# Kernel optimization log

Hardware: AMD Instinct MI355X
Metric: run time of the kernel (lower is better)

Reference implementation:

```python
import jax, jax.numpy as jnp
import numpy as np

B, A, C, G = 32, 5, 20, 19
TPER = 8  # targets per image -> T = B*TPER = 256
ANCHORS = np.array([[1.3221, 1.73145], [3.19275, 4.00944], [5.05587, 8.09892],
                    [9.47112, 4.84053], [11.2364, 10.0071]], dtype=np.float32)
OBJECT_SCALE, NOOBJECT_SCALE, CLASS_SCALE, COORD_SCALE = 5.0, 1.0, 1.0, 1.0
THRESH = 0.6


def _wh_iou_np(anc, wh):
    inter = np.minimum(anc[:, 0:1], wh[None, :, 0]) * np.minimum(anc[:, 1:2], wh[None, :, 1])
    union = anc[:, 0:1] * anc[:, 1:2] + wh[None, :, 0] * wh[None, :, 1] - inter
    return inter / (union + 1e-16)


def setup_inputs() -> dict:
    rng = np.random.default_rng(0)
    rows = []
    for b in range(B):
        cells = rng.choice(G * G, TPER, replace=False)  # distinct grid cells per image
        for c in cells:
            gy, gx = divmod(int(c), G)
            u, v = rng.uniform(0.05, 0.95, 2)
            w, h = rng.uniform(1.0, 8.0, 2) / G  # 1..8 grid units, in 0..1 image coords
            rows.append([b, rng.integers(C), (gx + u) / G, (gy + v) / G, w, h])
    t = np.array(rows, dtype=np.float32)
    # sort targets into (sample, anchor, gy, gx) mask order so mask-order gathers
    # line up with target-row order (as the original torch code implicitly assumes)
    wh_g = t[:, 4:6] * G
    ai = np.argmax(_wh_iou_np(ANCHORS, wh_g), axis=0)
    gx = (t[:, 2] * G).astype(np.int64)
    gy = (t[:, 3] * G).astype(np.int64)
    flat = ((t[:, 0].astype(np.int64) * A + ai) * G + gy) * G + gx
    t = t[np.argsort(flat)]
    x = jax.random.normal(jax.random.key(0), (B, A * (C + 5), G, G), dtype=jnp.float32) * 0.5
    return {"x": x, "targets": jnp.asarray(t), "seen": 0}


def _bbox_iou(b1, b2):
    # center-format boxes, last dim = (x, y, w, h); broadcasts over leading dims
    b1x1 = b1[..., 0] - b1[..., 2] / 2; b1x2 = b1[..., 0] + b1[..., 2] / 2
    b1y1 = b1[..., 1] - b1[..., 3] / 2; b1y2 = b1[..., 1] + b1[..., 3] / 2
    b2x1 = b2[..., 0] - b2[..., 2] / 2; b2x2 = b2[..., 0] + b2[..., 2] / 2
    b2y1 = b2[..., 1] - b2[..., 3] / 2; b2y2 = b2[..., 1] + b2[..., 3] / 2
    iw = jnp.clip(jnp.minimum(b1x2, b2x2) - jnp.maximum(b1x1, b2x1), 0.0)
    ih = jnp.clip(jnp.minimum(b1y2, b2y2) - jnp.maximum(b1y1, b2y1), 0.0)
    inter = iw * ih
    union = b1[..., 2] * b1[..., 3] + b2[..., 2] * b2[..., 3] - inter
    return inter / (union + 1e-16)


def _forward(x, targets, seen):
    anchors = jnp.asarray(ANCHORS)
    xp = x.reshape(B, A, C + 5, G, G).transpose(0, 1, 3, 4, 2)  # (B,A,G,G,C+5)
    tx, ty, tw, th = xp[..., 0], xp[..., 1], xp[..., 2], xp[..., 3]
    pred_conf = jax.nn.sigmoid(xp[..., 4])
    pred_cls = jax.nn.sigmoid(xp[..., 5:])
    tgs = targets[:, 2:6] * G  # (T,4) in grid units
    # anchor assignment via wh-iou (argmax over anchors)
    inter = jnp.minimum(anchors[:, 0:1], tgs[None, :, 2]) * jnp.minimum(anchors[:, 1:2], tgs[None, :, 3])
    wh_iou = inter / (anchors[:, 0:1] * anchors[:, 1:2] + tgs[None, :, 2] * tgs[None, :, 3] - inter)
    ai = jnp.argmax(wh_iou, axis=0)
    gx = tgs[:, 0].astype(jnp.int32); gy = tgs[:, 1].astype(jnp.int32)
    si = targets[:, 0].astype(jnp.int32); ci = targets[:, 1].astype(jnp.int32)
    # decode full grid
    gridx = jnp.arange(G, dtype=x.dtype)[None, None, None, :]
    gridy = jnp.arange(G, dtype=x.dtype)[None, None, :, None]
    sx, sy = jax.nn.sigmoid(tx), jax.nn.sigmoid(ty)
    pw = jnp.exp(tw) * anchors[:, 0][None, :, None, None]
    ph = jnp.exp(th) * anchors[:, 1][None, :, None, None]
    pred_boxes = jnp.stack([sx + gridx, sy + gridy, pw, ph], axis=-1)  # (B,A,G,G,4)
    T = targets.shape[0]
    target_mask = jnp.zeros((B, A, G, G), bool).at[si, ai, gy, gx].set(True)
    # losses at the T target locations (targets pre-sorted into mask order)
    iou_t = _bbox_iou(pred_boxes[si, ai, gy, gx], tgs)  # (T,)
    loss_cls = jnp.mean((pred_cls[si, ai, gy, gx] - jax.nn.one_hot(ci, C, dtype=x.dtype)) ** 2) * CLASS_SCALE
    tconf = iou_t  # rescore == 1: target_conf = 1 * iou
    loss_obj = jnp.mean((pred_conf[si, ai, gy, gx] - tconf) ** 2) * OBJECT_SCALE
    tcoords = jnp.stack([tgs[:, 0] - gx, tgs[:, 1] - gy,
                         jnp.log(tgs[:, 2] / anchors[ai, 0]),
                         jnp.log(tgs[:, 3] / anchors[ai, 1])], axis=-1)  # (T,4)
    pcoords_t = jnp.stack([sx[si, ai, gy, gx], sy[si, ai, gy, gx],
                           tw[si, ai, gy, gx], th[si, ai, gy, gx]], axis=-1)
    scale = jnp.sqrt(2.0 - tgs[:, 2] * tgs[:, 3] / (G * G))[:, None]
    loss_coords = jnp.mean(((pcoords_t - tcoords) * scale) ** 2) * COORD_SCALE
    # noobject mask: any-target IoU > thresh suppresses the noobj penalty (chunked over targets)
    CHUNK = 32
    tchunks = tgs.reshape(T // CHUNK, CHUNK, 4)
    def body(mx, tc):
        iou = _bbox_iou(pred_boxes[None], tc[:, None, None, None, None, :])  # (CHUNK,B,A,G,G)
        return jnp.maximum(mx, iou.max(0)), None
    max_iou, _ = jax.lax.scan(body, jnp.zeros((B, A, G, G), x.dtype), tchunks)
    noobj = (~target_mask) & (max_iou <= THRESH)
    ncnt = jnp.sum(noobj)
    loss_noobj = jnp.sum(jnp.where(noobj, pred_conf ** 2, 0.0)) / ncnt * NOOBJECT_SCALE
    total = loss_cls + loss_obj + loss_coords + loss_noobj
    if seen < 12800:
        prior = jnp.array([0.5, 0.5, 0.0, 0.0], x.dtype)
        pcoords = jnp.stack([sx, sy, tw, th], axis=-1)  # (B,A,G,G,4)
        nm = ~target_mask
        loss_prior = jnp.sum(jnp.where(nm[..., None], (pcoords - prior) ** 2, 0.0)) / (jnp.sum(nm) * 4) * 0.01
        total = total + loss_prior
    return total


def reference(x, targets, seen):
    return _forward(x, targets, seen)
```

## Files before the change

### kernel.cpp

```cpp
#include <hip/hip_runtime.h>
#include <math.h>

#define NB 32
#define NA 5
#define NC 20
#define NG 19
#define NT 256
#define GG  (NG*NG)
#define CELLS (NB*NA*NG*NG)
#define CPB 64
#define NBLK ((CELLS + CPB - 1)/CPB)
#define NWAVE 8
#define NTHR (NWAVE*64)

#define OBJECT_SCALE   5.0f
#define NOOBJ_SCALE    1.0f
#define CLASS_SCALE    1.0f
#define COORD_SCALE    1.0f

__constant__ float c_aw[5] = {1.3221f, 3.19275f, 5.05587f, 9.47112f, 11.2364f};
__constant__ float c_ah[5] = {1.73145f, 4.00944f, 8.09892f, 4.84053f, 10.0071f};

__device__ __forceinline__ float sigm(float v) { return 1.f / (1.f + expf(-v)); }

#define SUMS_OFF 0
#define PART_OFF 16

__global__ __launch_bounds__(NTHR)
void k_main(const float* __restrict__ x, const float* __restrict__ tg,
            float* __restrict__ ws_f, float* __restrict__ partials) {
    __shared__ float4 s_corn[NT];
    __shared__ float  s_s06[NT];
    __shared__ int    s_mask[CPB];
    __shared__ float  s_pm[NWAVE][CPB];
    __shared__ float  s_wred[12];

    const int t = threadIdx.x;
    const int wave = t >> 6, lane = t & 63;
    const int cellBase = blockIdx.x * CPB;
    const int idx = cellBase + lane;
    const bool valid = idx < CELLS;

    float txv = 0.f, tyv = 0.f, twv = 0.f, thv = 0.f, cfv = 0.f;
    int ca = 0, cgx = 0, cgy = 0;
    if (valid) {
        int gx = idx % NG;
        int r  = idx / NG;
        int gy = r % NG;  r /= NG;
        int a  = r % NA;
        int b  = r / NA;
        ca = a; cgx = gx; cgy = gy;
        int base = ((b*NA + a)*(NC+5))*GG + gy*NG + gx;
        txv = x[base + 0*GG];
        tyv = x[base + 1*GG];
        twv = x[base + 2*GG];
        thv = x[base + 3*GG];
        cfv = x[base + 4*GG];
    }
    if (t < CPB) s_mask[t] = 0;

    float gxf = 0.f, gyf = 0.f, gw = 0.f, gh = 0.f;
    int si = 0, ci = 0, ai = 0, gxi = 0, gyi = 0, fid = -1;
    if (t < NT) {
        const float2* tg2 = (const float2*)tg;
        float2 p0 = tg2[t*3+0], p1 = tg2[t*3+1], p2 = tg2[t*3+2];
        gxf = p1.x * NG; gyf = p1.y * NG;
        gw  = p2.x * NG; gh  = p2.y * NG;
        si = (int)p0.x; ci = (int)p0.y;
        float tarea = gw * gh;
        float b_inter = fminf(c_aw[0], gw) * fminf(c_ah[0], gh);
        float b_uni   = c_aw[0]*c_ah[0] + tarea - b_inter;
        #pragma unroll
        for (int a = 1; a < NA; ++a) {
            float inter = fminf(c_aw[a], gw) * fminf(c_ah[a], gh);
            float uni   = c_aw[a]*c_ah[a] + tarea - inter;
            if (inter * b_uni > b_inter * uni) { b_inter = inter; b_uni = uni; ai = a; }
        }
        gxi = (int)gxf; gyi = (int)gyf;
        fid = ((si*NA + ai)*NG + gyi)*NG + gxi;
        float hw = gw*0.5f, hh = gh*0.5f;
        s_corn[t] = make_float4(gxf - hw, gyf - hh, gxf + hw, gyf + hh);
        s_s06[t]  = 0.6f * tarea;
    }
    __syncthreads();

    if (t < NT) {
        int rel = fid - cellBase;
        if (rel >= 0 && rel < CPB) s_mask[rel] = 1;
    }
    float bx1 = 1e30f, by1 = 1e30f, bx2 = 1e30f, by2 = 1e30f, cthr = 0.f;
    float sx = 0.f, sy = 0.f;
    if (valid) {
        sx = sigm(txv); sy = sigm(tyv);
        float pw = expf(twv) * c_aw[ca], ph = expf(thv) * c_ah[ca];
        float cx = sx + (float)cgx, cy = sy + (float)cgy;
        bx1 = cx - pw*0.5f; bx2 = cx + pw*0.5f;
        by1 = cy - ph*0.5f; by2 = cy + ph*0.5f;
        cthr = 0.6f * (pw * ph) + 6e-17f;
    }
    __syncthreads();

    float m0 = -1e30f, m1 = -1e30f;
    #pragma unroll
    for (int i = 0; i < 16; ++i) {
        int j0 = (i << 4) + wave;
        int j1 = j0 + 8;
        float4 ta = s_corn[j0];
        float sa = s_s06[j0];
        float4 tb = s_corn[j1];
        float sb = s_s06[j1];
        float iwa = fmaxf(fminf(bx2, ta.z) - fmaxf(bx1, ta.x), 0.f);
        float iha = fmaxf(fminf(by2, ta.w) - fmaxf(by1, ta.y), 0.f);
        float iwb = fmaxf(fminf(bx2, tb.z) - fmaxf(bx1, tb.x), 0.f);
        float ihb = fmaxf(fminf(by2, tb.w) - fmaxf(by1, tb.y), 0.f);
        m0 = fmaxf(m0, fmaf(1.6f, iwa * iha, -sa));
        m1 = fmaxf(m1, fmaf(1.6f, iwb * ihb, -sb));
    }
    s_pm[wave][lane] = fmaxf(m0, m1);
    __syncthreads();

    if (wave == 0) {
        float mm = s_pm[0][lane];
        #pragma unroll
        for (int w = 1; w < NWAVE; ++w) mm = fmaxf(mm, s_pm[w][lane]);
        float v_no = 0.f, v_nc = 0.f, v_pr = 0.f, v_nm = 0.f;
        if (valid && !s_mask[lane]) {
            v_nm = 1.f;
            float e0 = sx - 0.5f, e1 = sy - 0.5f;
            v_pr = e0*e0 + e1*e1 + twv*twv + thv*thv;
            if (!(mm > cthr)) {
                float pc = sigm(cfv);
                v_no = pc * pc;
                v_nc = 1.f;
            }
        }
        #pragma unroll
        for (int off = 32; off > 0; off >>= 1) {
            v_no += __shfl_down(v_no, off);
            v_nc += __shfl_down(v_nc, off);
            v_pr += __shfl_down(v_pr, off);
            v_nm += __shfl_down(v_nm, off);
        }
        if (lane == 0) {
            partials[blockIdx.x*4 + 0] = v_no;
            partials[blockIdx.x*4 + 1] = v_nc;
            partials[blockIdx.x*4 + 2] = v_pr;
            partials[blockIdx.x*4 + 3] = v_nm;
        }
    }

    if (blockIdx.x == 0) {
        float s_cls = 0.f, s_obj = 0.f, s_crd = 0.f;
        if (t < NT) {
            int base = ((si*NA + ai)*(NC+5))*GG + gyi*NG + gxi;
            float txt = x[base + 0*GG];
            float tyt = x[base + 1*GG];
            float twt = x[base + 2*GG];
            float tht = x[base + 3*GG];
            float cft = x[base + 4*GG];
            float tsx = sigm(txt), tsy = sigm(tyt);
            float aw = c_aw[ai], ah = c_ah[ai];
            float pw = expf(twt) * aw, ph = expf(tht) * ah;

            float pcx = tsx + (float)gxi, pcy = tsy + (float)gyi;
            float hw = gw*0.5f, hh = gh*0.5f;
            float iw = fmaxf(0.f, fminf(pcx + pw*0.5f, gxf + hw) - fmaxf(pcx - pw*0.5f, gxf - hw));
            float ih = fmaxf(0.f, fminf(pcy + ph*0.5f, gyf + hh) - fmaxf(pcy - ph*0.5f, gyf - hh));
            float inter = iw * ih;
            float uni = pw*ph + gw*gh - inter;
            float iou = inter / (uni + 1e-16f);

            float pconf = sigm(cft);
            float dobj = pconf - iou;
            s_obj = dobj * dobj;

            for (int cc = 0; cc < NC; ++cc) {
                float pc = sigm(x[base + (5 + cc)*GG]);
                float d = pc - ((cc == ci) ? 1.f : 0.f);
                s_cls += d * d;
            }

            float scl = sqrtf(2.f - gw*gh / (float)(NG*NG));
            float d0 = (tsx - (gxf - (float)gxi)) * scl;
            float d1 = (tsy - (gyf - (float)gyi)) * scl;
            float d2 = (twt - logf(gw / aw)) * scl;
            float d3 = (tht - logf(gh / ah)) * scl;
            s_crd = d0*d0 + d1*d1 + d2*d2 + d3*d3;

            #pragma unroll
            for (int off = 32; off > 0; off >>= 1) {
                s_cls += __shfl_down(s_cls, off);
                s_obj += __shfl_down(s_obj, off);
                s_crd += __shfl_down(s_crd, off);
            }
            if (lane == 0) {
                s_wred[wave*3 + 0] = s_cls;
                s_wred[wave*3 + 1] = s_obj;
                s_wred[wave*3 + 2] = s_crd;
            }
        }
        __syncthreads();
        if (t == 0) {
            ws_f[SUMS_OFF + 0] = s_wred[0] + s_wred[3] + s_wred[6] + s_wred[9];
            ws_f[SUMS_OFF + 1] = s_wred[1] + s_wred[4] + s_wred[7] + s_wred[10];
            ws_f[SUMS_OFF + 2] = s_wred[2] + s_wred[5] + s_wred[8] + s_wred[11];
        }
    }
}

__global__ __launch_bounds__(256)
void k_final(const float* __restrict__ ws_f, const float* __restrict__ partials,
             const int* __restrict__ seen, float* __restrict__ out) {
    const float4* p4 = (const float4*)partials;
    int t = threadIdx.x;
    float a0 = 0.f, a1 = 0.f, a2 = 0.f, a3 = 0.f;
    for (int j = t; j < NBLK; j += 256) {
        float4 v = p4[j];
        a0 += v.x; a1 += v.y; a2 += v.z; a3 += v.w;
    }
    #pragma unroll
    for (int off = 32; off > 0; off >>= 1) {
        a0 += __shfl_down(a0, off);
        a1 += __shfl_down(a1, off);
        a2 += __shfl_down(a2, off);
        a3 += __shfl_down(a3, off);
    }
    __shared__ float s_w[4][4];
    int wave = t >> 6, lane = t & 63;
    if (lane == 0) {
        s_w[wave][0] = a0; s_w[wave][1] = a1; s_w[wave][2] = a2; s_w[wave][3] = a3;
    }
    __syncthreads();
    if (t == 0) {
        float r0 = s_w[0][0] + s_w[1][0] + s_w[2][0] + s_w[3][0];
        float r1 = s_w[0][1] + s_w[1][1] + s_w[2][1] + s_w[3][1];
        float r2 = s_w[0][2] + s_w[1][2] + s_w[2][2] + s_w[3][2];
        float r3 = s_w[0][3] + s_w[1][3] + s_w[2][3] + s_w[3][3];
        float loss_cls = ws_f[SUMS_OFF + 0] / (float)(NT * NC) * CLASS_SCALE;
        float loss_obj = ws_f[SUMS_OFF + 1] / (float)NT * OBJECT_SCALE;
        float loss_crd = ws_f[SUMS_OFF + 2] / (float)(NT * 4) * COORD_SCALE;
        float loss_no  = r0 / r1 * NOOBJ_SCALE;
        float total = loss_cls + loss_obj + loss_crd + loss_no;
        if (seen[0] < 12800) {
            total += r2 / (r3 * 4.f) * 0.01f;
        }
        out[0] = total;
    }
}

extern "C" void kernel_launch(void* const* d_in, const int* in_sizes, int n_in,
                              void* d_out, int out_size, void* d_ws, size_t ws_size,
                              hipStream_t stream) {
    const float* x    = (const float*)d_in[0];
    const float* tg   = (const float*)d_in[1];
    const int*   seen = (const int*)d_in[2];
    float* out  = (float*)d_out;
    float* ws_f = (float*)d_ws;
    float* partials = ws_f + PART_OFF;

    k_main<<<NBLK, NTHR, 0, stream>>>(x, tg, ws_f, partials);
    k_final<<<1, 256, 0, stream>>>(ws_f, partials, seen, out);
}
```

Before: 17.71 us.

## Process 128 cells per block with two wave groups splitting targets four ways

Each block now covers 128 grid cells instead of 64. The 8 waves form two groups of 4, and within a group each wave scans a quarter of the targets rather than an eighth. This halves the block count and the per-block setup work (loading target corners into shared memory, building the mask), and each block writes two partials. The cost is a longer IoU loop per thread and fewer blocks to spread across the GPU's compute units.

```diff
diff --git a/kernel.cpp b/kernel.cpp
--- a/kernel.cpp
+++ b/kernel.cpp
@@ -8,8 +8,9 @@
 #define NT 256
 #define GG  (NG*NG)
 #define CELLS (NB*NA*NG*NG)
-#define CPB 64
+#define CPB 128
 #define NBLK ((CELLS + CPB - 1)/CPB)
+#define NPART (NBLK*2)
 #define NWAVE 8
 #define NTHR (NWAVE*64)
 
@@ -32,13 +33,15 @@
     __shared__ float4 s_corn[NT];
     __shared__ float  s_s06[NT];
     __shared__ int    s_mask[CPB];
-    __shared__ float  s_pm[NWAVE][CPB];
+    __shared__ float  s_pm[4][CPB];
     __shared__ float  s_wred[12];
 
     const int t = threadIdx.x;
     const int wave = t >> 6, lane = t & 63;
+    const int grp = wave >> 2, sub = wave & 3;
+    const int cl  = lane + (grp << 6);
     const int cellBase = blockIdx.x * CPB;
-    const int idx = cellBase + lane;
+    const int idx = cellBase + cl;
     const bool valid = idx < CELLS;
 
     float txv = 0.f, tyv = 0.f, twv = 0.f, thv = 0.f, cfv = 0.f;
@@ -102,9 +105,9 @@
 
     float m0 = -1e30f, m1 = -1e30f;
     #pragma unroll
-    for (int i = 0; i < 16; ++i) {
-        int j0 = (i << 4) + wave;
-        int j1 = j0 + 8;
+    for (int i = 0; i < 32; ++i) {
+        int j0 = (i << 3) + sub;
+        int j1 = j0 + 4;
         float4 ta = s_corn[j0];
         float sa = s_s06[j0];
         float4 tb = s_corn[j1];
@@ -116,15 +119,14 @@
         m0 = fmaxf(m0, fmaf(1.6f, iwa * iha, -sa));
         m1 = fmaxf(m1, fmaf(1.6f, iwb * ihb, -sb));
     }
-    s_pm[wave][lane] = fmaxf(m0, m1);
-    __syncthreads();
-
-    if (wave == 0) {
-        float mm = s_pm[0][lane];
-        #pragma unroll
-        for (int w = 1; w < NWAVE; ++w) mm = fmaxf(mm, s_pm[w][lane]);
+    s_pm[sub][cl] = fmaxf(m0, m1);
+    __syncthreads();
+
+    if (sub == 0) {
+        float mm = fmaxf(fmaxf(s_pm[0][cl], s_pm[1][cl]),
+                         fmaxf(s_pm[2][cl], s_pm[3][cl]));
         float v_no = 0.f, v_nc = 0.f, v_pr = 0.f, v_nm = 0.f;
-        if (valid && !s_mask[lane]) {
+        if (valid && !s_mask[cl]) {
             v_nm = 1.f;
             float e0 = sx - 0.5f, e1 = sy - 0.5f;
             v_pr = e0*e0 + e1*e1 + twv*twv + thv*thv;
@@ -142,10 +144,11 @@
             v_nm += __shfl_down(v_nm, off);
         }
         if (lane == 0) {
-            partials[blockIdx.x*4 + 0] = v_no;
-            partials[blockIdx.x*4 + 1] = v_nc;
-            partials[blockIdx.x*4 + 2] = v_pr;
-            partials[blockIdx.x*4 + 3] = v_nm;
+            int p = blockIdx.x*2 + grp;
+            partials[p*4 + 0] = v_no;
+            partials[p*4 + 1] = v_nc;
+            partials[p*4 + 2] = v_pr;
+            partials[p*4 + 3] = v_nm;
         }
     }
 
@@ -214,7 +217,7 @@
     const float4* p4 = (const float4*)partials;
     int t = threadIdx.x;
     float a0 = 0.f, a1 = 0.f, a2 = 0.f, a3 = 0.f;
-    for (int j = t; j < NBLK; j += 256) {
+    for (int j = t; j < NPART; j += 256) {
         float4 v = p4[j];
         a0 += v.x; a1 += v.y; a2 += v.z; a3 += v.w;
     }
```

After: 17.28 us (median of 2 runs). -2.4%, faster.
